# Performance work log

Measured on AMD Instinct MI355X. Metric: run time of the kernel, lower is better.

Reference implementation:

```python
import jax, jax.numpy as jnp
from jax import lax
import numpy as np

B, C, H, W = 32, 3, 224, 224
NUM_CLASSES = 100
K = 3  # kernel size
OUT1 = 32


def _bn(x, g, b, m, v, eps=1e-5):
    # eval-mode batchnorm over channel dim of NCHW
    inv = g / jnp.sqrt(v + eps)
    return x * inv[None, :, None, None] + (b - m * inv)[None, :, None, None]


def _conv(x, w, pad=1):
    return lax.conv_general_dilated(
        x, w, (1, 1), ((pad, pad), (pad, pad)),
        dimension_numbers=('NCHW', 'OIHW', 'NCHW'))


def _maxpool2(x):
    return lax.reduce_window(x, -jnp.inf, lax.max, (1, 1, 2, 2), (1, 1, 2, 2), 'VALID')


def setup_inputs() -> dict:
    key = jax.random.key(0)
    ks = jax.random.split(key, 32)
    n = lambda k, s, sc=0.05: jax.random.normal(k, s, jnp.float32) * sc
    u = lambda k, s: jax.random.uniform(k, s, jnp.float32, 0.5, 1.5)
    inp = {
        'x': jax.random.normal(ks[0], (B, C, H, W), jnp.float32),
        # weight_gen MLP: Linear(3,128)->ReLU->Linear(128,256)->ReLU->Linear(256, 32*3*3*3)
        'w1': n(ks[1], (128, C)), 'b1': n(ks[2], (128,)),
        'w2': n(ks[3], (256, 128)), 'b2': n(ks[4], (256,)),
        'w3': n(ks[5], (OUT1 * C * K * K, 256)), 'b3': n(ks[6], (OUT1 * C * K * K,)),
        # bias_gen: Linear(3, 32)
        'wb': n(ks[7], (OUT1, C)), 'bb': n(ks[8], (OUT1,)),
        'conv2_w': n(ks[9], (64, 32, 3, 3)), 'conv2_b': n(ks[10], (64,)),
        'conv3_w': n(ks[11], (128, 64, 3, 3)), 'conv3_b': n(ks[12], (128,)),
        'bn1_g': 1.0 + n(ks[13], (32,)), 'bn1_b': n(ks[14], (32,)), 'bn1_m': n(ks[15], (32,)), 'bn1_v': u(ks[16], (32,)),
        'bn2_g': 1.0 + n(ks[17], (64,)), 'bn2_b': n(ks[18], (64,)), 'bn2_m': n(ks[19], (64,)), 'bn2_v': u(ks[20], (64,)),
        'bn3_g': 1.0 + n(ks[21], (128,)), 'bn3_b': n(ks[22], (128,)), 'bn3_m': n(ks[23], (128,)), 'bn3_v': u(ks[24], (128,)),
        'fc_w': n(ks[25], (NUM_CLASSES, 128)), 'fc_b': n(ks[26], (NUM_CLASSES,)),
    }
    return inp


def reference(x, w1, b1, w2, b2, w3, b3, wb, bb, conv2_w, conv2_b, conv3_w, conv3_b,
              bn1_g, bn1_b, bn1_m, bn1_v, bn2_g, bn2_b, bn2_m, bn2_v,
              bn3_g, bn3_b, bn3_m, bn3_v, fc_w, fc_b):
    Bx = x.shape[0]
    # DynamicConv2D: channel indicator is all-ones since C == max_in_channels
    ind = jnp.ones((Bx, C), x.dtype)
    h = jax.nn.relu(ind @ w1.T + b1)
    h = jax.nn.relu(h @ w2.T + b2)
    dyn_w = (h @ w3.T + b3).reshape(Bx, OUT1, C, K, K)  # per-sample [O,I,k,k]
    dyn_b = ind @ wb.T + bb                             # per-sample [O]
    # vmap over batch: one single-image conv per sample with its own weights
    y = jax.vmap(lambda xi, wi, bi: _conv(xi[None], wi)[0] + bi[:, None, None])(x, dyn_w, dyn_b)
    y = jax.nn.relu(_bn(y, bn1_g, bn1_b, bn1_m, bn1_v))
    y = _maxpool2(y)
    y = jax.nn.relu(_bn(_conv(y, conv2_w) + conv2_b[None, :, None, None], bn2_g, bn2_b, bn2_m, bn2_v))
    y = _maxpool2(y)
    y = jax.nn.relu(_bn(_conv(y, conv3_w) + conv3_b[None, :, None, None], bn3_g, bn3_b, bn3_m, bn3_v))
    y = y.mean(axis=(2, 3))  # AdaptiveAvgPool2d((1,1)) + flatten
    # dropout is identity in eval
    return y @ fc_w.T + fc_b
```

## Files before the change

### kernel.cpp

```cpp
#include <hip/hip_runtime.h>
#include <hip/hip_bf16.h>

#define BATCH 32
#define HW1 224

typedef __attribute__((ext_vector_type(8))) short short8;
typedef __attribute__((ext_vector_type(4))) float floatx4;

static __device__ __forceinline__ unsigned short f2bf(float f) {
    unsigned int u = __float_as_uint(f);
    unsigned int r = (u + 0x7fffu + ((u >> 16) & 1u)) >> 16;
    return (unsigned short)r;
}

__global__ __launch_bounds__(256) void gen_dynw_repack(
    const float* __restrict__ w1, const float* __restrict__ b1,
    const float* __restrict__ w2, const float* __restrict__ b2,
    const float* __restrict__ w3, const float* __restrict__ b3,
    const float* __restrict__ conv2_w, const float* __restrict__ conv3_w,
    const float* __restrict__ wb, const float* __restrict__ bb,
    const float* __restrict__ conv2_b, const float* __restrict__ conv3_b,
    const float* __restrict__ bn1_g, const float* __restrict__ bn1_b,
    const float* __restrict__ bn1_m, const float* __restrict__ bn1_v,
    const float* __restrict__ bn2_g, const float* __restrict__ bn2_b,
    const float* __restrict__ bn2_m, const float* __restrict__ bn2_v,
    const float* __restrict__ bn3_g, const float* __restrict__ bn3_b,
    const float* __restrict__ bn3_m, const float* __restrict__ bn3_v,
    float* __restrict__ dwt,
    unsigned short* __restrict__ wrep2, unsigned short* __restrict__ wrep3,
    float* __restrict__ bn1_s, float* __restrict__ bn1_t,
    float* __restrict__ bn2_s, float* __restrict__ bn2_t,
    float* __restrict__ bn3_s, float* __restrict__ bn3_t,
    float* __restrict__ feat)
{
    __shared__ float h1s[128];
    __shared__ float h2s[256];
    const int blk = blockIdx.x;
    const int t = threadIdx.x;
    if (blk < 216) {
        if (t < 128) {
            float s = b1[t] + w1[t*3+0] + w1[t*3+1] + w1[t*3+2];
            h1s[t] = fmaxf(s, 0.f);
        }
        __syncthreads();
        {
            float s = b2[t];
            const float* wr = w2 + (size_t)t*128;
#pragma unroll 4
            for (int k = 0; k < 128; k += 4) {
                float4 wv = *(const float4*)(wr + k);
                s = fmaf(wv.x, h1s[k  ], s);
                s = fmaf(wv.y, h1s[k+1], s);
                s = fmaf(wv.z, h1s[k+2], s);
                s = fmaf(wv.w, h1s[k+3], s);
            }
            h2s[t] = fmaxf(s, 0.f);
        }
        __syncthreads();
        const int wave = t >> 6, lane = t & 63;
        const int row = blk*4 + wave;
        float4 wv = *(const float4*)(w3 + (size_t)row*256 + lane*4);
        float4 hv = *(const float4*)&h2s[lane*4];
        float s = wv.x*hv.x + wv.y*hv.y + wv.z*hv.z + wv.w*hv.w;
#pragma unroll
        for (int m = 1; m < 64; m <<= 1) s += __shfl_xor(s, m);
        if (lane == 0) {
            int oc = row / 27, tap = row - oc*27;
            dwt[tap*32 + oc] = s + b3[row];
        }
    } else if (blk < 576) {
        const int i = (blk - 216)*256 + t;
        const int N2 = 9*64*32;
        if (i < N2) {
            int tp = i / (64*32); int rem = i - tp*(64*32);
            int oc = rem >> 5, ic = rem & 31;
            wrep2[i] = f2bf(conv2_w[(oc*32 + ic)*9 + tp]);
        } else {
            int j = i - N2;
            int tp = j / (128*64); int rem = j - tp*(128*64);
            int oc = rem >> 6, ic = rem & 63;
            wrep3[j] = f2bf(conv3_w[(oc*64 + ic)*9 + tp]);
        }
    } else {
        if (t < 32) {
            float dynb = bb[t] + wb[t*3+0] + wb[t*3+1] + wb[t*3+2];
            float s = bn1_g[t] / sqrtf(bn1_v[t] + 1e-5f);
            bn1_s[t] = s;
            bn1_t[t] = (dynb - bn1_m[t]) * s + bn1_b[t];
        }
        if (t < 64) {
            float s = bn2_g[t] / sqrtf(bn2_v[t] + 1e-5f);
            bn2_s[t] = s;
            bn2_t[t] = (conv2_b[t] - bn2_m[t]) * s + bn2_b[t];
        }
        if (t < 128) {
            float s = bn3_g[t] / sqrtf(bn3_v[t] + 1e-5f);
            bn3_s[t] = s;
            bn3_t[t] = (conv3_b[t] - bn3_m[t]) * s + bn3_b[t];
        }
        for (int i = t; i < BATCH*128; i += 256) feat[i] = 0.f;
    }
}

__global__ __launch_bounds__(256) void conv1_pool(
    const float* __restrict__ x, const float* __restrict__ dwt,
    const float* __restrict__ bn_s, const float* __restrict__ bn_t,
    unsigned short* __restrict__ act1)
{
    __shared__ __align__(16) unsigned short sp[18*18*4];
    __shared__ __align__(16) unsigned short swA[32*32];
    __shared__ __align__(16) unsigned short swB[32*32];

    const int tid = threadIdx.x;
    const int bx = blockIdx.x, by = blockIdx.y, b = blockIdx.z;
    const int gx0 = bx*16 - 1, gy0 = by*16 - 1;
    const float* xb = x + (size_t)b * 3 * HW1 * HW1;

    for (int i = tid; i < 1024; i += 256) { swA[i] = 0; swB[i] = 0; }

    for (int i = tid; i < 324; i += 256) {
        int r = i / 18, c = i - r*18;
        int gy = gy0 + r, gx = gx0 + c;
        unsigned short v0 = 0, v1 = 0, v2 = 0;
        if ((unsigned)gy < HW1 && (unsigned)gx < HW1) {
            const float* pp = xb + gy*HW1 + gx;
            v0 = f2bf(pp[0]);
            v1 = f2bf(pp[HW1*HW1]);
            v2 = f2bf(pp[2*HW1*HW1]);
        }
        unsigned int lo = (unsigned int)v0 | ((unsigned int)v1 << 16);
        unsigned int hi = (unsigned int)v2;
        *(uint2*)&sp[i*4] = make_uint2(lo, hi);
    }
    __syncthreads();

    for (int i = tid; i < 864; i += 256) {
        int tap = i >> 5, oc = i & 31;
        int ic = tap / 9, kk = tap - ic*9;
        int ky = kk / 3, kx = kk - ky*3;
        unsigned short v = f2bf(dwt[i]);
        if (kk == 8)      swB[oc*32 + ic] = v;
        else if (kx < 2)  swA[oc*32 + ky*8 + kx*4 + ic] = v;
        else              swA[oc*32 + 3*8  + ky*4 + ic] = v;
    }
    __syncthreads();

    const int lane = tid & 63, wave = tid >> 6;
    const int n = lane & 15, quad = lane >> 4;

    short8 afrA[2], afrB[2];
#pragma unroll
    for (int h = 0; h < 2; ++h) {
        afrA[h] = *(const short8*)&swA[((h*16 + n)*32) + quad*8];
        afrB[h] = *(const short8*)&swB[((h*16 + n)*32) + quad*8];
    }
    float4 sv[2], tv[2];
#pragma unroll
    for (int h = 0; h < 2; ++h) {
        sv[h] = *(const float4*)(bn_s + h*16 + quad*4);
        tv[h] = *(const float4*)(bn_t + h*16 + quad*4);
    }

    union U { short8 s8; uint2 u2[2]; };

    const int y0w = wave*4;
    float ev[2][4];

#pragma unroll
    for (int yi = 0; yi < 4; ++yi) {
        const int y = y0w + yi;
        int r0 = (quad < 3) ? (y + quad) : y;
        int c0 = (quad < 3) ? n : (n + 2);
        int r1 = (quad < 3) ? (y + quad) : (y + 1);
        int c1 = (quad < 3) ? (n + 1) : (n + 2);
        U bf1;
        bf1.u2[0] = *(const uint2*)&sp[(r0*18 + c0)*4];
        bf1.u2[1] = *(const uint2*)&sp[(r1*18 + c1)*4];
        U bf2;
        bf2.u2[0] = *(const uint2*)&sp[((y+2)*18 + (n+2))*4];
        bf2.u2[1] = bf2.u2[0];

        float vr[2][4];
#pragma unroll
        for (int h = 0; h < 2; ++h) {
            floatx4 acc = {0.f, 0.f, 0.f, 0.f};
            acc = __builtin_amdgcn_mfma_f32_16x16x32_bf16(afrA[h], bf1.s8, acc, 0, 0, 0);
            acc = __builtin_amdgcn_mfma_f32_16x16x32_bf16(afrB[h], bf2.s8, acc, 0, 0, 0);
            float sj[4] = {sv[h].x, sv[h].y, sv[h].z, sv[h].w};
            float tj[4] = {tv[h].x, tv[h].y, tv[h].z, tv[h].w};
#pragma unroll
            for (int j = 0; j < 4; ++j)
                vr[h][j] = fmaxf(fmaf(acc[j], sj[j], tj[j]), 0.f);
        }

        if ((yi & 1) == 0) {
#pragma unroll
            for (int h = 0; h < 2; ++h)
#pragma unroll
                for (int j = 0; j < 4; ++j) ev[h][j] = vr[h][j];
        } else {
            int py = by*8 + ((y0w + yi) >> 1);
            int px = bx*8 + (n >> 1);
            unsigned short* dstp =
                act1 + ((size_t)((b*112 + py)*112 + px))*32 + quad*4;
#pragma unroll
            for (int h = 0; h < 2; ++h) {
                unsigned int pk[2];
#pragma unroll
                for (int j = 0; j < 4; ++j) {
                    float m = fmaxf(vr[h][j], ev[h][j]);
                    m = fmaxf(m, __shfl_xor(m, 1));
                    unsigned short us = f2bf(m);
                    if (j & 1) pk[j >> 1] |= ((unsigned int)us) << 16;
                    else       pk[j >> 1]  = us;
                }
                if (!(n & 1)) *(uint2*)(dstp + h*16) = *(uint2*)pk;
            }
        }
    }
}

__global__ __launch_bounds__(256) void conv2_mfma(
    const unsigned short* __restrict__ act1,
    const unsigned short* __restrict__ wrep,
    const float* __restrict__ bn_s, const float* __restrict__ bn_t,
    unsigned short* __restrict__ act2)
{
    constexpr int IC = 32, OC = 64, H = 112;
    __shared__ __align__(16) short lds[4*18*18*8];

    const int tid = threadIdx.x;
    const int b = blockIdx.z;
    const int cx0 = blockIdx.x*16, cy0 = blockIdx.y*16;
    const unsigned short* ab = act1 + (size_t)b*H*H*IC;

    for (int s = tid; s < 4*324; s += 256) {
        int ck = s / 324; int rem = s - ck*324;
        int y = rem / 18, xx = rem - y*18;
        int gy = cy0 - 1 + y, gx = cx0 - 1 + xx;
        uint4 v = {0,0,0,0};
        if ((unsigned)gy < H && (unsigned)gx < H)
            v = *(const uint4*)(ab + (size_t)(gy*H + gx)*IC + ck*8);
        *(uint4*)&lds[s*8] = v;
    }

    const int lane = tid & 63, wave = tid >> 6;
    const int n = lane & 15, quad = lane >> 4;
    const int oc0w = wave * 16;

    short8 afr[9];
#pragma unroll
    for (int t = 0; t < 9; ++t)
        afr[t] = *(const short8*)(wrep + (size_t)(t*OC + oc0w + n)*IC + quad*8);

    float4 sv = *(const float4*)(bn_s + oc0w + quad*4);
    float4 tv = *(const float4*)(bn_t + oc0w + quad*4);
    float sj[4] = {sv.x, sv.y, sv.z, sv.w};
    float tj[4] = {tv.x, tv.y, tv.z, tv.w};

    __syncthreads();

    floatx4 acc[3];
    float ev[4];

#pragma unroll
    for (int r = 0; r < 18; ++r) {
        const short* rp = &lds[((quad*18 + r)*18 + n)*8];
        short8 w0 = *(const short8*)(rp);
        short8 w1 = *(const short8*)(rp + 8);
        short8 w2 = *(const short8*)(rp + 16);

        if (r < 16) {
            floatx4 a = {0.f,0.f,0.f,0.f};
            a = __builtin_amdgcn_mfma_f32_16x16x32_bf16(afr[0], w0, a, 0, 0, 0);
            a = __builtin_amdgcn_mfma_f32_16x16x32_bf16(afr[1], w1, a, 0, 0, 0);
            a = __builtin_amdgcn_mfma_f32_16x16x32_bf16(afr[2], w2, a, 0, 0, 0);
            acc[r % 3] = a;
        }
        if (r >= 1 && r <= 16) {
            int y = r - 1;
            floatx4 a = acc[y % 3];
            a = __builtin_amdgcn_mfma_f32_16x16x32_bf16(afr[3], w0, a, 0, 0, 0);
            a = __builtin_amdgcn_mfma_f32_16x16x32_bf16(afr[4], w1, a, 0, 0, 0);
            a = __builtin_amdgcn_mfma_f32_16x16x32_bf16(afr[5], w2, a, 0, 0, 0);
            acc[y % 3] = a;
        }
        if (r >= 2) {
            int y = r - 2;
            floatx4 a = acc[y % 3];
            a = __builtin_amdgcn_mfma_f32_16x16x32_bf16(afr[6], w0, a, 0, 0, 0);
            a = __builtin_amdgcn_mfma_f32_16x16x32_bf16(afr[7], w1, a, 0, 0, 0);
            a = __builtin_amdgcn_mfma_f32_16x16x32_bf16(afr[8], w2, a, 0, 0, 0);

            float v[4];
#pragma unroll
            for (int j = 0; j < 4; ++j)
                v[j] = fmaxf(fmaf(a[j], sj[j], tj[j]), 0.f);

            if ((y & 1) == 0) {
#pragma unroll
                for (int j = 0; j < 4; ++j) ev[j] = v[j];
            } else {
                unsigned int pk[2];
#pragma unroll
                for (int j = 0; j < 4; ++j) {
                    float m = fmaxf(v[j], ev[j]);
                    m = fmaxf(m, __shfl_xor(m, 1));
                    unsigned short us = f2bf(m);
                    if (j & 1) pk[j >> 1] |= ((unsigned int)us) << 16;
                    else       pk[j >> 1]  = us;
                }
                if (!(n & 1)) {
                    int py = (cy0 >> 1) + (y >> 1), px = (cx0 >> 1) + (n >> 1);
                    unsigned short* dstp =
                        act2 + ((size_t)((b*56 + py)*56 + px))*OC + oc0w + quad*4;
                    *(uint2*)dstp = *(uint2*)pk;
                }
            }
        }
    }
}

__global__ __launch_bounds__(256) void conv3_mfma(
    const unsigned short* __restrict__ act2,
    const unsigned short* __restrict__ wrep,
    const float* __restrict__ bn_s, const float* __restrict__ bn_t,
    float* __restrict__ feat)
{
    constexpr int IC = 64, OC = 128, H = 56;
    __shared__ __align__(16) short lds[8*18*18*8];

    const int tid = threadIdx.x;
    const int b = blockIdx.z >> 1, half = blockIdx.z & 1;
    const int cx0 = blockIdx.x*16, cy0 = blockIdx.y*16;
    const unsigned short* ab = act2 + (size_t)b*H*H*IC;

    for (int s = tid; s < 8*324; s += 256) {
        int ck = s / 324; int rem = s - ck*324;
        int y = rem / 18, xx = rem - y*18;
        int gy = cy0 - 1 + y, gx = cx0 - 1 + xx;
        uint4 v = {0,0,0,0};
        if ((unsigned)gy < H && (unsigned)gx < H)
            v = *(const uint4*)(ab + (size_t)(gy*H + gx)*IC + ck*8);
        *(uint4*)&lds[s*8] = v;
    }

    const int lane = tid & 63, wave = tid >> 6;
    const int n = lane & 15, quad = lane >> 4;
    const int oc0w = half*64 + wave*16;

    short8 afr[18];
#pragma unroll
    for (int t = 0; t < 9; ++t)
#pragma unroll
        for (int kc = 0; kc < 2; ++kc)
            afr[t*2 + kc] = *(const short8*)(wrep + (size_t)(t*OC + oc0w + n)*IC + kc*32 + quad*8);

    float4 sv = *(const float4*)(bn_s + oc0w + quad*4);
    float4 tv = *(const float4*)(bn_t + oc0w + quad*4);

    __syncthreads();

    float sum[4] = {0.f, 0.f, 0.f, 0.f};
    const bool vx = (cx0 + n) < H;
    const int ymax = (H - cy0) < 16 ? (H - cy0) : 16;
    float sj[4] = {sv.x, sv.y, sv.z, sv.w};
    float tj[4] = {tv.x, tv.y, tv.z, tv.w};

    for (int y = 0; y < ymax; ++y) {
        floatx4 acc0 = {0.f,0.f,0.f,0.f};
        floatx4 acc1 = {0.f,0.f,0.f,0.f};
#pragma unroll
        for (int ky = 0; ky < 3; ++ky)
#pragma unroll
            for (int kx = 0; kx < 3; ++kx) {
                int t = ky*3 + kx;
                short8 b0 = *(const short8*)&lds[(((0*4 + quad)*18 + y+ky)*18 + n+kx)*8];
                short8 b1 = *(const short8*)&lds[(((1*4 + quad)*18 + y+ky)*18 + n+kx)*8];
                acc0 = __builtin_amdgcn_mfma_f32_16x16x32_bf16(afr[t*2+0], b0, acc0, 0, 0, 0);
                acc1 = __builtin_amdgcn_mfma_f32_16x16x32_bf16(afr[t*2+1], b1, acc1, 0, 0, 0);
            }
        if (vx) {
#pragma unroll
            for (int j = 0; j < 4; ++j)
                sum[j] += fmaxf(fmaf(acc0[j] + acc1[j], sj[j], tj[j]), 0.f);
        }
    }
#pragma unroll
    for (int j = 0; j < 4; ++j) {
        sum[j] += __shfl_xor(sum[j], 1);
        sum[j] += __shfl_xor(sum[j], 2);
        sum[j] += __shfl_xor(sum[j], 4);
        sum[j] += __shfl_xor(sum[j], 8);
    }
    if (n == 0) {
#pragma unroll
        for (int j = 0; j < 4; ++j)
            atomicAdd(&feat[b*128 + oc0w + quad*4 + j], sum[j]);
    }
}

__global__ __launch_bounds__(256) void fc_kernel(
    const float* __restrict__ feat, const float* __restrict__ fc_w,
    const float* __restrict__ fc_b, float* __restrict__ out)
{
    int i = blockIdx.x * 256 + threadIdx.x;
    if (i >= BATCH*100) return;
    int b = i / 100, n = i - b*100;
    const float* f = feat + b*128;
    const float* w = fc_w + n*128;
    float s = 0.f;
#pragma unroll 4
    for (int k = 0; k < 128; ++k) s = fmaf(f[k], w[k], s);
    out[i] = s * (1.f/3136.f) + fc_b[n];
}

extern "C" void kernel_launch(void* const* d_in, const int* in_sizes, int n_in,
                              void* d_out, int out_size, void* d_ws, size_t ws_size,
                              hipStream_t stream)
{
    const float* x       = (const float*)d_in[0];
    const float* w1      = (const float*)d_in[1];
    const float* b1      = (const float*)d_in[2];
    const float* w2      = (const float*)d_in[3];
    const float* b2      = (const float*)d_in[4];
    const float* w3      = (const float*)d_in[5];
    const float* b3      = (const float*)d_in[6];
    const float* wb      = (const float*)d_in[7];
    const float* bb      = (const float*)d_in[8];
    const float* conv2_w = (const float*)d_in[9];
    const float* conv2_b = (const float*)d_in[10];
    const float* conv3_w = (const float*)d_in[11];
    const float* conv3_b = (const float*)d_in[12];
    const float* bn1_g = (const float*)d_in[13];
    const float* bn1_b = (const float*)d_in[14];
    const float* bn1_m = (const float*)d_in[15];
    const float* bn1_v = (const float*)d_in[16];
    const float* bn2_g = (const float*)d_in[17];
    const float* bn2_b = (const float*)d_in[18];
    const float* bn2_m = (const float*)d_in[19];
    const float* bn2_v = (const float*)d_in[20];
    const float* bn3_g = (const float*)d_in[21];
    const float* bn3_b = (const float*)d_in[22];
    const float* bn3_m = (const float*)d_in[23];
    const float* bn3_v = (const float*)d_in[24];
    const float* fc_w  = (const float*)d_in[25];
    const float* fc_b  = (const float*)d_in[26];
    float* out = (float*)d_out;

    char* wsb = (char*)d_ws;
    float* ws    = (float*)d_ws;
    float* dwt   = ws;
    float* bn1_s = ws + 864;
    float* bn1_t = ws + 896;
    float* bn2_s = ws + 928;
    float* bn2_t = ws + 992;
    float* bn3_s = ws + 1056;
    float* bn3_t = ws + 1184;
    float* feat  = ws + 1312;
    unsigned short* wrep2 = (unsigned short*)(wsb + 32768);
    unsigned short* wrep3 = (unsigned short*)(wsb + 69632);
    unsigned short* act1  = (unsigned short*)(wsb + 262144);
    unsigned short* act2  = (unsigned short*)(wsb + 262144 + 25690112);

    gen_dynw_repack<<<577, 256, 0, stream>>>(
        w1, b1, w2, b2, w3, b3, conv2_w, conv3_w,
        wb, bb, conv2_b, conv3_b,
        bn1_g, bn1_b, bn1_m, bn1_v, bn2_g, bn2_b, bn2_m, bn2_v,
        bn3_g, bn3_b, bn3_m, bn3_v,
        dwt, wrep2, wrep3,
        bn1_s, bn1_t, bn2_s, bn2_t, bn3_s, bn3_t, feat);

    conv1_pool<<<dim3(14, 14, BATCH), 256, 0, stream>>>(
        x, dwt, bn1_s, bn1_t, act1);

    conv2_mfma<<<dim3(7, 7, BATCH), 256, 0, stream>>>(
        act1, wrep2, bn2_s, bn2_t, act2);

    conv3_mfma<<<dim3(4, 4, BATCH*2), 256, 0, stream>>>(
        act2, wrep3, bn3_s, bn3_t, feat);

    fc_kernel<<<(BATCH*100 + 255)/256, 256, 0, stream>>>(feat, fc_w, fc_b, out);
}
```

Measured before the change: 200.3 us.

## Reuse each LDS input row across three output rows in conv3 MFMA loop

```diff
diff --git a/kernel.cpp b/kernel.cpp
--- a/kernel.cpp
+++ b/kernel.cpp
@@ -328,15 +328,15 @@
     float* __restrict__ feat)
 {
     constexpr int IC = 64, OC = 128, H = 56;
-    __shared__ __align__(16) short lds[8*18*18*8];
+    __shared__ __align__(16) short lds[8*16*18*8];
 
     const int tid = threadIdx.x;
     const int b = blockIdx.z >> 1, half = blockIdx.z & 1;
-    const int cx0 = blockIdx.x*16, cy0 = blockIdx.y*16;
+    const int cx0 = blockIdx.x*16, cy0 = blockIdx.y*14;
     const unsigned short* ab = act2 + (size_t)b*H*H*IC;
 
-    for (int s = tid; s < 8*324; s += 256) {
-        int ck = s / 324; int rem = s - ck*324;
+    for (int s = tid; s < 8*16*18; s += 256) {
+        int ck = s / (16*18); int rem = s - ck*(16*18);
         int y = rem / 18, xx = rem - y*18;
         int gy = cy0 - 1 + y, gx = cx0 - 1 + xx;
         uint4 v = {0,0,0,0};
@@ -358,32 +358,61 @@
 
     float4 sv = *(const float4*)(bn_s + oc0w + quad*4);
     float4 tv = *(const float4*)(bn_t + oc0w + quad*4);
+    float sj[4] = {sv.x, sv.y, sv.z, sv.w};
+    float tj[4] = {tv.x, tv.y, tv.z, tv.w};
 
     __syncthreads();
 
     float sum[4] = {0.f, 0.f, 0.f, 0.f};
     const bool vx = (cx0 + n) < H;
-    const int ymax = (H - cy0) < 16 ? (H - cy0) : 16;
-    float sj[4] = {sv.x, sv.y, sv.z, sv.w};
-    float tj[4] = {tv.x, tv.y, tv.z, tv.w};
-
-    for (int y = 0; y < ymax; ++y) {
-        floatx4 acc0 = {0.f,0.f,0.f,0.f};
-        floatx4 acc1 = {0.f,0.f,0.f,0.f};
-#pragma unroll
-        for (int ky = 0; ky < 3; ++ky)
-#pragma unroll
-            for (int kx = 0; kx < 3; ++kx) {
-                int t = ky*3 + kx;
-                short8 b0 = *(const short8*)&lds[(((0*4 + quad)*18 + y+ky)*18 + n+kx)*8];
-                short8 b1 = *(const short8*)&lds[(((1*4 + quad)*18 + y+ky)*18 + n+kx)*8];
-                acc0 = __builtin_amdgcn_mfma_f32_16x16x32_bf16(afr[t*2+0], b0, acc0, 0, 0, 0);
-                acc1 = __builtin_amdgcn_mfma_f32_16x16x32_bf16(afr[t*2+1], b1, acc1, 0, 0, 0);
+    floatx4 acc[3];
+
+#pragma unroll
+    for (int r = 0; r < 16; ++r) {
+        const short* p0 = &lds[((quad*16     + r)*18 + n)*8];
+        const short* p1 = &lds[(((4+quad)*16 + r)*18 + n)*8];
+        short8 a0 = *(const short8*)(p0);
+        short8 a1 = *(const short8*)(p0 + 8);
+        short8 a2 = *(const short8*)(p0 + 16);
+        short8 b0 = *(const short8*)(p1);
+        short8 b1 = *(const short8*)(p1 + 8);
+        short8 b2 = *(const short8*)(p1 + 16);
+
+        if (r < 14) {
+            floatx4 a = {0.f,0.f,0.f,0.f};
+            a = __builtin_amdgcn_mfma_f32_16x16x32_bf16(afr[0], a0, a, 0, 0, 0);
+            a = __builtin_amdgcn_mfma_f32_16x16x32_bf16(afr[1], b0, a, 0, 0, 0);
+            a = __builtin_amdgcn_mfma_f32_16x16x32_bf16(afr[2], a1, a, 0, 0, 0);
+            a = __builtin_amdgcn_mfma_f32_16x16x32_bf16(afr[3], b1, a, 0, 0, 0);
+            a = __builtin_amdgcn_mfma_f32_16x16x32_bf16(afr[4], a2, a, 0, 0, 0);
+            a = __builtin_amdgcn_mfma_f32_16x16x32_bf16(afr[5], b2, a, 0, 0, 0);
+            acc[r % 3] = a;
+        }
+        if (r >= 1 && r <= 14) {
+            int y = r - 1;
+            floatx4 a = acc[y % 3];
+            a = __builtin_amdgcn_mfma_f32_16x16x32_bf16(afr[6],  a0, a, 0, 0, 0);
+            a = __builtin_amdgcn_mfma_f32_16x16x32_bf16(afr[7],  b0, a, 0, 0, 0);
+            a = __builtin_amdgcn_mfma_f32_16x16x32_bf16(afr[8],  a1, a, 0, 0, 0);
+            a = __builtin_amdgcn_mfma_f32_16x16x32_bf16(afr[9],  b1, a, 0, 0, 0);
+            a = __builtin_amdgcn_mfma_f32_16x16x32_bf16(afr[10], a2, a, 0, 0, 0);
+            a = __builtin_amdgcn_mfma_f32_16x16x32_bf16(afr[11], b2, a, 0, 0, 0);
+            acc[y % 3] = a;
+        }
+        if (r >= 2) {
+            int y = r - 2;
+            floatx4 a = acc[y % 3];
+            a = __builtin_amdgcn_mfma_f32_16x16x32_bf16(afr[12], a0, a, 0, 0, 0);
+            a = __builtin_amdgcn_mfma_f32_16x16x32_bf16(afr[13], b0, a, 0, 0, 0);
+            a = __builtin_amdgcn_mfma_f32_16x16x32_bf16(afr[14], a1, a, 0, 0, 0);
+            a = __builtin_amdgcn_mfma_f32_16x16x32_bf16(afr[15], b1, a, 0, 0, 0);
+            a = __builtin_amdgcn_mfma_f32_16x16x32_bf16(afr[16], a2, a, 0, 0, 0);
+            a = __builtin_amdgcn_mfma_f32_16x16x32_bf16(afr[17], b2, a, 0, 0, 0);
+            if (vx) {
+#pragma unroll
+                for (int j = 0; j < 4; ++j)
+                    sum[j] += fmaxf(fmaf(a[j], sj[j], tj[j]), 0.f);
             }
-        if (vx) {
-#pragma unroll
-            for (int j = 0; j < 4; ++j)
-                sum[j] += fmaxf(fmaf(acc0[j] + acc1[j], sj[j], tj[j]), 0.f);
         }
     }
 #pragma unroll
```

After: 190.4 us. -5.0%, faster.
